# Kernel tuning notes

Hardware: AMD Instinct MI355X
Metric: run time of the kernel (lower is better)

## Reference

```python
import jax, jax.numpy as jnp
import numpy as np


def position_encoding(feature_size, d_model):
    pos = jnp.arange(feature_size, dtype=jnp.float32)[:, None]
    _2i = jnp.arange(0, d_model, 2, dtype=jnp.float32)
    ang = pos / jnp.power(10000.0, _2i / d_model)  # [F, D/2]
    pe = jnp.zeros((feature_size, d_model), dtype=jnp.float32)
    pe = pe.at[:, 0::2].set(jnp.sin(ang))
    pe = pe.at[:, 1::2].set(jnp.cos(ang))
    return pe


def setup_inputs() -> dict:
    key = jax.random.key(0)
    ks = jax.random.split(key, 11)
    B, F, D, T, V = 32, 512, 256, 32, 128
    sc = 0.02
    return {
        "f": jax.random.normal(ks[0], (B, F, D), dtype=jnp.float32),
        "decoder_input_ids": jax.random.randint(ks[1], (B, T), 0, V),
        "emb": sc * jax.random.normal(ks[2], (V, D), dtype=jnp.float32),
        "w_e": sc * jax.random.normal(ks[3], (D, D), dtype=jnp.float32),
        "w_h": sc * jax.random.normal(ks[4], (D, D), dtype=jnp.float32),
        "w_f": sc * jax.random.normal(ks[5], (D, D), dtype=jnp.float32),
        "w_q": sc * jax.random.normal(ks[6], (D, D), dtype=jnp.float32),
        "w_s": sc * jax.random.normal(ks[7], (D, D), dtype=jnp.float32),
        "w_g": sc * jax.random.normal(ks[8], (D, 2 * D), dtype=jnp.float32),
        "w_ih": sc * jax.random.normal(ks[9], (4 * D, 2 * D), dtype=jnp.float32),
        "w_hh": sc * jax.random.normal(ks[10], (4 * D, D), dtype=jnp.float32),
    }


def reference(f, decoder_input_ids, emb, w_e, w_h, w_f, w_q, w_s, w_g, w_ih, w_hh):
    B, F, D = f.shape
    q = position_encoding(F, D)                      # [F, D]
    dec = emb[decoder_input_ids]                     # [B, T, D]
    # loop-invariant attention terms, hoisted: w_f(f) + w_q(q)
    base = jnp.einsum('bfd,od->bfo', f, w_f) + (q @ w_q.T)[None]  # [B, F, D]
    fq = f + q[None]                                 # [B, F, D]

    def step(carry, x_t):
        h, cell, s, cp = carry
        # LSTMCell (bias=False), torch gate order i, f, g, o
        xin = jnp.concatenate([x_t, cp], axis=-1)    # [B, 2D]
        gates = xin @ w_ih.T + h @ w_hh.T            # [B, 4D]
        gi, gf, gg, go = jnp.split(gates, 4, axis=-1)
        cell = jax.nn.sigmoid(gf) * cell + jax.nn.sigmoid(gi) * jnp.tanh(gg)
        h = jax.nn.sigmoid(go) * jnp.tanh(cell)
        # Bahdanau-style energy; softmax over feature (last) dim per source
        t_in = jnp.tanh((h @ w_h.T)[:, None] + base + jnp.einsum('bfd,od->bfo', s, w_s))
        e = jnp.einsum('bfd,od->bfo', t_in, w_e)     # [B, F, D]
        alpha = jax.nn.softmax(e, axis=-1)
        s = s + alpha
        c = (alpha * f).sum(1)                       # [B, D]
        cp = (alpha * fq).sum(1)                     # [B, D]
        pred = jnp.concatenate([c, h], axis=-1) @ w_g.T  # [B, D]
        return (h, cell, s, cp), pred

    z = jnp.zeros((B, D), dtype=f.dtype)
    carry0 = (z, z, jnp.zeros_like(f), z)
    _, preds = jax.lax.scan(step, carry0, jnp.swapaxes(dec, 0, 1))  # [T, B, D]
    return jnp.swapaxes(preds, 0, 1)                 # [B, T, D]
```

## Files before the change

### kernel.cpp

```cpp
#include <hip/hip_runtime.h>
#include <math.h>

#define NB 32
#define NF 512
#define ND 256
#define NT 32
#define RPB 32
#define NTILE (NF / RPB)

typedef __attribute__((ext_vector_type(8))) short bf16x8;
typedef __attribute__((ext_vector_type(4))) float f32x4;

__device__ __forceinline__ float sigmoidf_(float x) { return 1.0f / (1.0f + __expf(-x)); }

__device__ __forceinline__ short f2bf(float x) {
    union { float f; unsigned u; } v; v.f = x;
    unsigned r = (v.u + 0x7FFF + ((v.u >> 16) & 1)) >> 16;
    return (short)r;
}

__global__ void pe_kernel(float* __restrict__ q) {
    int p = blockIdx.x;
    int d = threadIdx.x;
    float i2 = (float)((d >> 1) << 1);
    float rate = expf(-9.210340371976184f * (i2 / (float)ND));
    float ang = (float)p * rate;
    q[p * ND + d] = (d & 1) ? cosf(ang) : sinf(ang);
}

__global__ void gather_kernel(const int* __restrict__ ids, const float* __restrict__ emb,
                              float* __restrict__ dec) {
    int bt = blockIdx.x;
    int d = threadIdx.x;
    dec[(size_t)bt * ND + d] = emb[(size_t)ids[bt] * ND + d];
}

__global__ void wcvt_kernel(const float* __restrict__ w, short* __restrict__ wb, int n) {
    int i = blockIdx.x * 256 + threadIdx.x;
    if (i < n) wb[i] = f2bf(w[i]);
}

__global__ void qwq_kernel(const float* __restrict__ q, const float* __restrict__ w_q,
                           float* __restrict__ qwq) {
    int p = blockIdx.x;
    int o = threadIdx.x;
    __shared__ float qs[ND];
    qs[o] = q[(size_t)p * ND + o];
    __syncthreads();
    const float4* wr = (const float4*)(w_q + (size_t)o * ND);
    float acc = 0.f;
    for (int k4 = 0; k4 < ND / 4; ++k4) {
        float4 w = wr[k4];
        int k = 4 * k4;
        acc += qs[k] * w.x + qs[k + 1] * w.y + qs[k + 2] * w.z + qs[k + 3] * w.w;
    }
    qwq[(size_t)p * ND + o] = acc;
}

__global__ void base_kernel(const float* __restrict__ fin, const float* __restrict__ w_f,
                            const float* __restrict__ qwq, float* __restrict__ bsum) {
    int b = blockIdx.x / NTILE;
    int f0 = (blockIdx.x % NTILE) * RPB;
    int o = threadIdx.x;
    __shared__ float fs[RPB][ND];
    #pragma unroll
    for (int r = 0; r < RPB; ++r)
        fs[r][o] = fin[((size_t)(b * NF + f0 + r)) * ND + o];
    __syncthreads();
    float acc[RPB];
    #pragma unroll
    for (int r = 0; r < RPB; ++r) acc[r] = 0.f;
    const float4* wr = (const float4*)(w_f + (size_t)o * ND);
    for (int k4 = 0; k4 < ND / 4; ++k4) {
        float4 w = wr[k4];
        int k = 4 * k4;
        #pragma unroll
        for (int r = 0; r < RPB; ++r)
            acc[r] += fs[r][k] * w.x + fs[r][k + 1] * w.y + fs[r][k + 2] * w.z + fs[r][k + 3] * w.w;
    }
    #pragma unroll
    for (int r = 0; r < RPB; ++r)
        bsum[((size_t)(b * NF + f0 + r)) * ND + o] = acc[r] + qwq[(size_t)(f0 + r) * ND + o];
}

#define ZSTRIDE 769
#define ZPSTRIDE 513
__global__ void gates_kernel(int t, int mode,
                             const float* __restrict__ dec,
                             const float* __restrict__ cpart, const float* __restrict__ cppart,
                             const float* __restrict__ h,
                             const float* __restrict__ w_ih, const float* __restrict__ w_hh,
                             const float* __restrict__ w_g,
                             float* __restrict__ gatesT, float* __restrict__ out) {
    extern __shared__ float lds[];
    int bid = blockIdx.x;
    int tid = threadIdx.x;

    if (bid < 128) {
        if (!(mode & 1)) return;
        int j0 = bid * 8;
        float* wl = lds;
        float* zl = lds + 8 * 768;
        float4* wl4 = (float4*)wl;
        for (int cc = 0; cc < 6; ++cc) {
            int idx4 = tid + cc * 256;
            int flat = idx4 * 4;
            int r = flat / 768;
            int col = flat - r * 768;
            float4 v;
            if (col < 512) v = *(const float4*)(w_ih + (size_t)(j0 + r) * 512 + col);
            else           v = *(const float4*)(w_hh + (size_t)(j0 + r) * 256 + (col - 512));
            wl4[idx4] = v;
        }
        for (int b = 0; b < NB; ++b) {
            int d = tid;
            float xv = (t < NT) ? dec[((size_t)b * NT + t) * ND + d] : 0.f;
            float cpsum = 0.f;
            if (t > 0) {
                #pragma unroll
                for (int tl = 0; tl < NTILE; ++tl)
                    cpsum += cppart[((size_t)tl * NB + b) * ND + d];
            }
            float hv = h[(size_t)b * ND + d];
            zl[b * ZSTRIDE + d]       = xv;
            zl[b * ZSTRIDE + 256 + d] = cpsum;
            zl[b * ZSTRIDE + 512 + d] = hv;
        }
        __syncthreads();
        int r = tid >> 5;
        int b = tid & 31;
        const float4* wr4 = (const float4*)(wl + r * 768);
        const float* zb = zl + b * ZSTRIDE;
        float acc = 0.f;
        #pragma unroll 8
        for (int k4 = 0; k4 < 192; ++k4) {
            float4 w = wr4[k4];
            int k = 4 * k4;
            acc += w.x * zb[k] + w.y * zb[k + 1] + w.z * zb[k + 2] + w.w * zb[k + 3];
        }
        gatesT[(size_t)b * 1024 + (j0 + r)] = acc;
    } else {
        if (!(mode & 2)) return;
        int p0 = (bid - 128) * 8;
        float* wl = lds;
        float* zl = lds + 8 * 512;
        float4* wl4 = (float4*)wl;
        for (int cc = 0; cc < 4; ++cc) {
            int idx4 = tid + cc * 256;
            int flat = idx4 * 4;
            int r = flat >> 9;
            int col = flat & 511;
            wl4[idx4] = *(const float4*)(w_g + (size_t)(p0 + r) * 512 + col);
        }
        for (int b = 0; b < NB; ++b) {
            float csum = 0.f;
            #pragma unroll
            for (int tl = 0; tl < NTILE; ++tl)
                csum += cpart[((size_t)tl * NB + b) * ND + tid];
            zl[b * ZPSTRIDE + tid]       = csum;
            zl[b * ZPSTRIDE + 256 + tid] = h[(size_t)b * ND + tid];
        }
        __syncthreads();
        int r = tid >> 5;
        int b = tid & 31;
        const float4* wr4 = (const float4*)(wl + r * 512);
        const float* zb = zl + b * ZPSTRIDE;
        float acc = 0.f;
        #pragma unroll 8
        for (int k4 = 0; k4 < 128; ++k4) {
            float4 w = wr4[k4];
            int k = 4 * k4;
            acc += w.x * zb[k] + w.y * zb[k + 1] + w.z * zb[k + 2] + w.w * zb[k + 3];
        }
        out[((size_t)b * NT + (t - 1)) * ND + p0 + r] = acc;
    }
}

__global__ void __launch_bounds__(256) attn_step_kernel(
        float* __restrict__ bsum,
        const float* __restrict__ fin, const float* __restrict__ q,
        const float* __restrict__ gatesT,
        const float* __restrict__ cell_prev, float* __restrict__ cell_next,
        float* __restrict__ h_next,
        const float* __restrict__ w_h,
        const short* __restrict__ w_e_bf, const short* __restrict__ w_s_bf,
        float* __restrict__ cpart, float* __restrict__ cppart) {
    int b = blockIdx.x / NTILE;
    int tile = blockIdx.x % NTILE;
    int f0 = tile * RPB;
    int tid = threadIdx.x;
    int l = tid & 63;
    int wv = tid >> 6;

    __shared__ __align__(16) short tin_bf[RPB * ND];
    __shared__ float xfer[RPB * 257];
    __shared__ float hn[ND];
    __shared__ float sred[RPB][5];

    int o0 = wv * 64;
    int c15 = l & 15;
    int g = l >> 4;
    char* tb = (char*)tin_bf;

    {
        float gi = gatesT[(size_t)b * 1024 + tid];
        float gf = gatesT[(size_t)b * 1024 + 256 + tid];
        float gg = gatesT[(size_t)b * 1024 + 512 + tid];
        float go = gatesT[(size_t)b * 1024 + 768 + tid];
        float cold = cell_prev[(size_t)b * ND + tid];
        float cnew = sigmoidf_(gf) * cold + sigmoidf_(gi) * tanhf(gg);
        float hval = sigmoidf_(go) * tanhf(cnew);
        if (tile == 0) {
            cell_next[(size_t)b * ND + tid] = cnew;
            h_next[(size_t)b * ND + tid] = hval;
        }
        hn[tid] = hval;
    }
    __syncthreads();
    float hwh_reg = 0.f;
    {
        const float4* whr = (const float4*)(w_h + (size_t)tid * ND);
        #pragma unroll 8
        for (int k4 = 0; k4 < ND / 4; ++k4) {
            float4 w = whr[k4]; int k = 4 * k4;
            hwh_reg += hn[k] * w.x + hn[k + 1] * w.y + hn[k + 2] * w.z + hn[k + 3] * w.w;
        }
    }

    float bsv[RPB];
    #pragma unroll
    for (int r = 0; r < RPB; ++r) {
        float bs = bsum[((size_t)(b * NF + f0 + r)) * ND + tid];
        bsv[r] = bs;
        int byte = (r * 512 + tid * 2) ^ ((r & 7) << 4);
        *(short*)(tb + byte) = f2bf(tanhf(hwh_reg + bs));
    }
    __syncthreads();

    f32x4 acc[2][4];
    #pragma unroll
    for (int mt = 0; mt < 2; ++mt)
        #pragma unroll
        for (int nt = 0; nt < 4; ++nt)
            acc[mt][nt] = (f32x4)0.f;
    #pragma unroll
    for (int ks = 0; ks < 8; ++ks) {
        int kb = ks * 32 + g * 8;
        bf16x8 afr[2];
        #pragma unroll
        for (int mt = 0; mt < 2; ++mt) {
            int row = mt * 16 + c15;
            int byte = (row * 512 + kb * 2) ^ ((row & 7) << 4);
            afr[mt] = *(const bf16x8*)(tb + byte);
        }
        #pragma unroll
        for (int nt = 0; nt < 4; ++nt) {
            int o = o0 + nt * 16 + c15;
            bf16x8 bfr = *(const bf16x8*)(w_e_bf + (size_t)o * ND + kb);
            #pragma unroll
            for (int mt = 0; mt < 2; ++mt)
                acc[mt][nt] = __builtin_amdgcn_mfma_f32_16x16x32_bf16(afr[mt], bfr, acc[mt][nt], 0, 0, 0);
        }
    }

    {
        float ps[2][4];
        #pragma unroll
        for (int mt = 0; mt < 2; ++mt)
            #pragma unroll
            for (int reg = 0; reg < 4; ++reg) ps[mt][reg] = 0.f;
        #pragma unroll
        for (int mt = 0; mt < 2; ++mt)
            #pragma unroll
            for (int nt = 0; nt < 4; ++nt)
                #pragma unroll
                for (int reg = 0; reg < 4; ++reg) {
                    float a = __expf(acc[mt][nt][reg]);
                    acc[mt][nt][reg] = a;
                    ps[mt][reg] += a;
                }
        #pragma unroll
        for (int off = 1; off <= 8; off <<= 1)
            #pragma unroll
            for (int mt = 0; mt < 2; ++mt)
                #pragma unroll
                for (int reg = 0; reg < 4; ++reg)
                    ps[mt][reg] += __shfl_xor(ps[mt][reg], off);
        if (c15 == 0) {
            #pragma unroll
            for (int mt = 0; mt < 2; ++mt)
                #pragma unroll
                for (int reg = 0; reg < 4; ++reg)
                    sred[mt * 16 + g * 4 + reg][wv] = ps[mt][reg];
        }
        __syncthreads();
        #pragma unroll
        for (int mt = 0; mt < 2; ++mt)
            #pragma unroll
            for (int reg = 0; reg < 4; ++reg) {
                int r = mt * 16 + g * 4 + reg;
                float inv = 1.0f / (sred[r][0] + sred[r][1] + sred[r][2] + sred[r][3]);
                #pragma unroll
                for (int nt = 0; nt < 4; ++nt)
                    acc[mt][nt][reg] *= inv;
            }
    }

    #pragma unroll
    for (int mt = 0; mt < 2; ++mt)
        #pragma unroll
        for (int reg = 0; reg < 4; ++reg) {
            int r = mt * 16 + g * 4 + reg;
            #pragma unroll
            for (int nt = 0; nt < 4; ++nt)
                xfer[r * 257 + o0 + nt * 16 + c15] = acc[mt][nt][reg];
        }
    __syncthreads();

    {
        float pc = 0.f, pcp = 0.f;
        #pragma unroll
        for (int r = 0; r < RPB; ++r) {
            float a = xfer[r * 257 + tid];
            float fv = fin[((size_t)(b * NF + f0 + r)) * ND + tid];
            float qv = q[(size_t)(f0 + r) * ND + tid];
            pc += a * fv;
            pcp += a * (fv + qv);
            int byte = (r * 512 + tid * 2) ^ ((r & 7) << 4);
            *(short*)(tb + byte) = f2bf(a);
        }
        cpart [((size_t)tile * NB + b) * ND + tid] = pc;
        cppart[((size_t)tile * NB + b) * ND + tid] = pcp;
    }
    __syncthreads();

    {
        f32x4 acc2[2][4];
        #pragma unroll
        for (int mt = 0; mt < 2; ++mt)
            #pragma unroll
            for (int nt = 0; nt < 4; ++nt)
                acc2[mt][nt] = (f32x4)0.f;
        #pragma unroll
        for (int ks = 0; ks < 8; ++ks) {
            int kb = ks * 32 + g * 8;
            bf16x8 afr[2];
            #pragma unroll
            for (int mt = 0; mt < 2; ++mt) {
                int row = mt * 16 + c15;
                int byte = (row * 512 + kb * 2) ^ ((row & 7) << 4);
                afr[mt] = *(const bf16x8*)(tb + byte);
            }
            #pragma unroll
            for (int nt = 0; nt < 4; ++nt) {
                int o = o0 + nt * 16 + c15;
                bf16x8 bfr = *(const bf16x8*)(w_s_bf + (size_t)o * ND + kb);
                #pragma unroll
                for (int mt = 0; mt < 2; ++mt)
                    acc2[mt][nt] = __builtin_amdgcn_mfma_f32_16x16x32_bf16(afr[mt], bfr, acc2[mt][nt], 0, 0, 0);
            }
        }
        #pragma unroll
        for (int mt = 0; mt < 2; ++mt)
            #pragma unroll
            for (int reg = 0; reg < 4; ++reg) {
                int r = mt * 16 + g * 4 + reg;
                #pragma unroll
                for (int nt = 0; nt < 4; ++nt)
                    xfer[r * 257 + o0 + nt * 16 + c15] = acc2[mt][nt][reg];
            }
    }
    __syncthreads();

    #pragma unroll
    for (int r = 0; r < RPB; ++r)
        bsum[((size_t)(b * NF + f0 + r)) * ND + tid] = bsv[r] + xfer[r * 257 + tid];
}

extern "C" void kernel_launch(void* const* d_in, const int* in_sizes, int n_in,
                              void* d_out, int out_size, void* d_ws, size_t ws_size,
                              hipStream_t stream) {
    const float* fin  = (const float*)d_in[0];
    const int*   ids  = (const int*)  d_in[1];
    const float* emb  = (const float*)d_in[2];
    const float* w_e  = (const float*)d_in[3];
    const float* w_h  = (const float*)d_in[4];
    const float* w_f  = (const float*)d_in[5];
    const float* w_q  = (const float*)d_in[6];
    const float* w_s  = (const float*)d_in[7];
    const float* w_g  = (const float*)d_in[8];
    const float* w_ih = (const float*)d_in[9];
    const float* w_hh = (const float*)d_in[10];
    float* out = (float*)d_out;
    float* ws  = (float*)d_ws;

    size_t off = 0;
    float* q      = ws + off; off += (size_t)NF * ND;
    float* scratch= ws + off; off += (size_t)NF * ND;
    float* dec    = ws + off; off += (size_t)NB * NT * ND;
    float* bsum   = ws + off; off += (size_t)NB * NF * ND;
    float* h0     = ws + off; off += (size_t)NB * ND;
    float* h1     = ws + off; off += (size_t)NB * ND;
    float* cell0  = ws + off; off += (size_t)NB * ND;
    float* cell1  = ws + off; off += (size_t)NB * ND;
    float* cpart  = ws + off; off += (size_t)NTILE * NB * ND;
    float* cppart = ws + off; off += (size_t)NTILE * NB * ND;
    short* w_e_bf = (short*)(ws + off); off += (size_t)ND * ND / 2;
    short* w_s_bf = (short*)(ws + off); off += (size_t)ND * ND / 2;

    float* qwq    = scratch;
    float* gatesT = scratch;

    float* hbuf[2]    = { h0, h1 };
    float* cellbuf[2] = { cell0, cell1 };

    hipMemsetAsync(h0, 0, sizeof(float) * NB * ND, stream);
    hipMemsetAsync(cell0, 0, sizeof(float) * NB * ND, stream);

    pe_kernel<<<NF, ND, 0, stream>>>(q);
    gather_kernel<<<NB * NT, ND, 0, stream>>>(ids, emb, dec);
    wcvt_kernel<<<ND * ND / 256, 256, 0, stream>>>(w_e, w_e_bf, ND * ND);
    wcvt_kernel<<<ND * ND / 256, 256, 0, stream>>>(w_s, w_s_bf, ND * ND);
    qwq_kernel<<<NF, ND, 0, stream>>>(q, w_q, qwq);
    base_kernel<<<NB * NTILE, ND, 0, stream>>>(fin, w_f, qwq, bsum);

    const size_t gates_lds = (size_t)(8 * 768 + NB * ZSTRIDE) * sizeof(float);

    for (int t = 0; t < NT; ++t) {
        int mode = (t > 0) ? 3 : 1;
        int p = t & 1;
        gates_kernel<<<160, ND, gates_lds, stream>>>(t, mode, dec, cpart, cppart, hbuf[p],
                                                     w_ih, w_hh, w_g, gatesT, out);
        attn_step_kernel<<<NB * NTILE, ND, 0, stream>>>(bsum, fin, q, gatesT,
                                                        cellbuf[p], cellbuf[p ^ 1], hbuf[p ^ 1],
                                                        w_h, w_e_bf, w_s_bf, cpart, cppart);
    }
    gates_kernel<<<160, ND, gates_lds, stream>>>(NT, 2, dec, cpart, cppart, hbuf[0],
                                                 w_ih, w_hh, w_g, gatesT, out);
}
```

Measured before the change: 2.676 ms.

## Vectorize attention step epilogues, transpose w_h/w_g, restructure output projection and gather

Many changes at once. The embedding gather kernel is removed and the gates kernel reads emb by id directly. w_h and w_g are pre-transposed so h@w_h and the output projection read coalesced columns, and the output-projection blocks now cover one batch row each instead of 8 output rows. The attention step kernel gets float4 loads and stores for bsum, f and q, a 4-wave LDS reduction for the context sums, a padded xfer stride, launch bounds allowing 2 blocks per SM, and a separate gatesT buffer instead of aliasing the qwq scratch. The aim is fewer uncoalesced scalar accesses and higher occupancy, at the cost of more LDS and a few extra syncs.

After: 2.680 ms. No clear change (+0.2%).

```diff
diff --git a/kernel.cpp b/kernel.cpp
--- a/kernel.cpp
+++ b/kernel.cpp
@@ -7,8 +7,10 @@
 #define NT 32
 #define RPB 32
 #define NTILE (NF / RPB)
+#define XS 260
 
 typedef __attribute__((ext_vector_type(8))) short bf16x8;
+typedef __attribute__((ext_vector_type(4))) short bf16x4;
 typedef __attribute__((ext_vector_type(4))) float f32x4;
 
 __device__ __forceinline__ float sigmoidf_(float x) { return 1.0f / (1.0f + __expf(-x)); }
@@ -28,16 +30,17 @@
     q[p * ND + d] = (d & 1) ? cosf(ang) : sinf(ang);
 }
 
-__global__ void gather_kernel(const int* __restrict__ ids, const float* __restrict__ emb,
-                              float* __restrict__ dec) {
-    int bt = blockIdx.x;
-    int d = threadIdx.x;
-    dec[(size_t)bt * ND + d] = emb[(size_t)ids[bt] * ND + d];
-}
-
 __global__ void wcvt_kernel(const float* __restrict__ w, short* __restrict__ wb, int n) {
     int i = blockIdx.x * 256 + threadIdx.x;
     if (i < n) wb[i] = f2bf(w[i]);
+}
+
+__global__ void wprep_kernel(const float* __restrict__ w_h, const float* __restrict__ w_g,
+                             float* __restrict__ w_hT, float* __restrict__ w_gT) {
+    int k = blockIdx.x;
+    int o = threadIdx.x;
+    if (k < ND) w_hT[(size_t)k * ND + o] = w_h[(size_t)o * ND + k];
+    w_gT[(size_t)k * ND + o] = w_g[(size_t)o * 512 + k];
 }
 
 __global__ void qwq_kernel(const float* __restrict__ q, const float* __restrict__ w_q,
@@ -84,13 +87,12 @@
 }
 
 #define ZSTRIDE 769
-#define ZPSTRIDE 513
 __global__ void gates_kernel(int t, int mode,
-                             const float* __restrict__ dec,
+                             const int* __restrict__ ids, const float* __restrict__ emb,
                              const float* __restrict__ cpart, const float* __restrict__ cppart,
                              const float* __restrict__ h,
                              const float* __restrict__ w_ih, const float* __restrict__ w_hh,
-                             const float* __restrict__ w_g,
+                             const float* __restrict__ w_gT,
                              float* __restrict__ gatesT, float* __restrict__ out) {
     extern __shared__ float lds[];
     int bid = blockIdx.x;
@@ -114,7 +116,7 @@
         }
         for (int b = 0; b < NB; ++b) {
             int d = tid;
-            float xv = (t < NT) ? dec[((size_t)b * NT + t) * ND + d] : 0.f;
+            float xv = (t < NT) ? emb[(size_t)ids[b * NT + t] * ND + d] : 0.f;
             float cpsum = 0.f;
             if (t > 0) {
                 #pragma unroll
@@ -141,48 +143,30 @@
         gatesT[(size_t)b * 1024 + (j0 + r)] = acc;
     } else {
         if (!(mode & 2)) return;
-        int p0 = (bid - 128) * 8;
-        float* wl = lds;
-        float* zl = lds + 8 * 512;
-        float4* wl4 = (float4*)wl;
-        for (int cc = 0; cc < 4; ++cc) {
-            int idx4 = tid + cc * 256;
-            int flat = idx4 * 4;
-            int r = flat >> 9;
-            int col = flat & 511;
-            wl4[idx4] = *(const float4*)(w_g + (size_t)(p0 + r) * 512 + col);
-        }
-        for (int b = 0; b < NB; ++b) {
-            float csum = 0.f;
-            #pragma unroll
-            for (int tl = 0; tl < NTILE; ++tl)
-                csum += cpart[((size_t)tl * NB + b) * ND + tid];
-            zl[b * ZPSTRIDE + tid]       = csum;
-            zl[b * ZPSTRIDE + 256 + tid] = h[(size_t)b * ND + tid];
-        }
+        int b = bid - 128;
+        float* zp = lds;
+        float csum = 0.f;
+        #pragma unroll
+        for (int tl = 0; tl < NTILE; ++tl)
+            csum += cpart[((size_t)tl * NB + b) * ND + tid];
+        zp[tid] = csum;
+        zp[256 + tid] = h[(size_t)b * ND + tid];
         __syncthreads();
-        int r = tid >> 5;
-        int b = tid & 31;
-        const float4* wr4 = (const float4*)(wl + r * 512);
-        const float* zb = zl + b * ZPSTRIDE;
-        float acc = 0.f;
+        float p = 0.f;
         #pragma unroll 8
-        for (int k4 = 0; k4 < 128; ++k4) {
-            float4 w = wr4[k4];
-            int k = 4 * k4;
-            acc += w.x * zb[k] + w.y * zb[k + 1] + w.z * zb[k + 2] + w.w * zb[k + 3];
-        }
-        out[((size_t)b * NT + (t - 1)) * ND + p0 + r] = acc;
-    }
-}
-
-__global__ void __launch_bounds__(256) attn_step_kernel(
+        for (int k = 0; k < 512; ++k)
+            p += zp[k] * w_gT[(size_t)k * ND + tid];
+        out[((size_t)b * NT + (t - 1)) * ND + tid] = p;
+    }
+}
+
+__global__ void __launch_bounds__(256, 2) attn_step_kernel(
         float* __restrict__ bsum,
-        const float* __restrict__ fin, const float* __restrict__ q,
+        const float* __restrict__ fin, const float* __restrict__ qpe,
         const float* __restrict__ gatesT,
         const float* __restrict__ cell_prev, float* __restrict__ cell_next,
         float* __restrict__ h_next,
-        const float* __restrict__ w_h,
+        const float* __restrict__ w_hT,
         const short* __restrict__ w_e_bf, const short* __restrict__ w_s_bf,
         float* __restrict__ cpart, float* __restrict__ cppart) {
     int b = blockIdx.x / NTILE;
@@ -191,16 +175,18 @@
     int tid = threadIdx.x;
     int l = tid & 63;
     int wv = tid >> 6;
-
-    __shared__ __align__(16) short tin_bf[RPB * ND];
-    __shared__ float xfer[RPB * 257];
-    __shared__ float hn[ND];
-    __shared__ float sred[RPB][5];
-
-    int o0 = wv * 64;
     int c15 = l & 15;
     int g = l >> 4;
+    int c = l;
+    int o0 = wv * 64;
+
+    __shared__ __align__(16) short tin_bf[RPB * ND];
+    __shared__ float xfer[RPB * XS];
+    __shared__ float cred[2][1024];
+    __shared__ float sred[RPB][5];
     char* tb = (char*)tin_bf;
+    float* hn = xfer;
+    float* hwhl = xfer + 256;
 
     {
         float gi = gatesT[(size_t)b * 1024 + tid];
@@ -217,23 +203,29 @@
         hn[tid] = hval;
     }
     __syncthreads();
-    float hwh_reg = 0.f;
-    {
-        const float4* whr = (const float4*)(w_h + (size_t)tid * ND);
+    {
+        float a = 0.f;
         #pragma unroll 8
-        for (int k4 = 0; k4 < ND / 4; ++k4) {
-            float4 w = whr[k4]; int k = 4 * k4;
-            hwh_reg += hn[k] * w.x + hn[k + 1] * w.y + hn[k + 2] * w.z + hn[k + 3] * w.w;
-        }
-    }
-
-    float bsv[RPB];
-    #pragma unroll
-    for (int r = 0; r < RPB; ++r) {
-        float bs = bsum[((size_t)(b * NF + f0 + r)) * ND + tid];
-        bsv[r] = bs;
-        int byte = (r * 512 + tid * 2) ^ ((r & 7) << 4);
-        *(short*)(tb + byte) = f2bf(tanhf(hwh_reg + bs));
+        for (int k = 0; k < ND; ++k)
+            a += hn[k] * w_hT[(size_t)k * ND + tid];
+        hwhl[tid] = a;
+    }
+    __syncthreads();
+
+    float4 bsv4[8];
+    {
+        float4 hwh4 = *(const float4*)&hwhl[4 * c];
+        #pragma unroll
+        for (int i = 0; i < 8; ++i) {
+            int r = wv + 4 * i;
+            bsv4[i] = *(const float4*)(bsum + ((size_t)(b * NF + f0 + r)) * ND + 4 * c);
+            bf16x4 tv;
+            tv.x = f2bf(tanhf(hwh4.x + bsv4[i].x));
+            tv.y = f2bf(tanhf(hwh4.y + bsv4[i].y));
+            tv.z = f2bf(tanhf(hwh4.z + bsv4[i].z));
+            tv.w = f2bf(tanhf(hwh4.w + bsv4[i].w));
+            *(bf16x4*)(tb + ((r * 512 + 8 * c) ^ ((r & 7) << 4))) = tv;
+        }
     }
     __syncthreads();
 
@@ -250,8 +242,7 @@
         #pragma unroll
         for (int mt = 0; mt < 2; ++mt) {
             int row = mt * 16 + c15;
-            int byte = (row * 512 + kb * 2) ^ ((row & 7) << 4);
-            afr[mt] = *(const bf16x8*)(tb + byte);
+            afr[mt] = *(const bf16x8*)(tb + ((row * 512 + kb * 2) ^ ((row & 7) << 4)));
         }
         #pragma unroll
         for (int nt = 0; nt < 4; ++nt) {
@@ -313,26 +304,37 @@
             int r = mt * 16 + g * 4 + reg;
             #pragma unroll
             for (int nt = 0; nt < 4; ++nt)
-                xfer[r * 257 + o0 + nt * 16 + c15] = acc[mt][nt][reg];
-        }
-    __syncthreads();
-
-    {
-        float pc = 0.f, pcp = 0.f;
-        #pragma unroll
-        for (int r = 0; r < RPB; ++r) {
-            float a = xfer[r * 257 + tid];
-            float fv = fin[((size_t)(b * NF + f0 + r)) * ND + tid];
-            float qv = q[(size_t)(f0 + r) * ND + tid];
-            pc += a * fv;
-            pcp += a * (fv + qv);
-            int byte = (r * 512 + tid * 2) ^ ((r & 7) << 4);
-            *(short*)(tb + byte) = f2bf(a);
-        }
+                xfer[r * XS + o0 + nt * 16 + c15] = acc[mt][nt][reg];
+        }
+    __syncthreads();
+
+    {
+        float4 pc4 = {0.f, 0.f, 0.f, 0.f}, pcp4 = {0.f, 0.f, 0.f, 0.f};
+        #pragma unroll
+        for (int i = 0; i < 8; ++i) {
+            int r = wv + 4 * i;
+            float4 a4 = *(const float4*)&xfer[r * XS + 4 * c];
+            float4 f4 = *(const float4*)(fin + ((size_t)(b * NF + f0 + r)) * ND + 4 * c);
+            float4 q4 = *(const float4*)(qpe + ((size_t)(f0 + r)) * ND + 4 * c);
+            pc4.x += a4.x * f4.x;  pcp4.x += a4.x * (f4.x + q4.x);
+            pc4.y += a4.y * f4.y;  pcp4.y += a4.y * (f4.y + q4.y);
+            pc4.z += a4.z * f4.z;  pcp4.z += a4.z * (f4.z + q4.z);
+            pc4.w += a4.w * f4.w;  pcp4.w += a4.w * (f4.w + q4.w);
+            bf16x4 av;
+            av.x = f2bf(a4.x); av.y = f2bf(a4.y); av.z = f2bf(a4.z); av.w = f2bf(a4.w);
+            *(bf16x4*)(tb + ((r * 512 + 8 * c) ^ ((r & 7) << 4))) = av;
+        }
+        *(float4*)&cred[0][wv * 256 + 4 * c] = pc4;
+        *(float4*)&cred[1][wv * 256 + 4 * c] = pcp4;
+    }
+    __syncthreads();
+
+    {
+        float pc  = cred[0][tid] + cred[0][256 + tid] + cred[0][512 + tid] + cred[0][768 + tid];
+        float pcp = cred[1][tid] + cred[1][256 + tid] + cred[1][512 + tid] + cred[1][768 + tid];
         cpart [((size_t)tile * NB + b) * ND + tid] = pc;
         cppart[((size_t)tile * NB + b) * ND + tid] = pcp;
     }
-    __syncthreads();
 
     {
         f32x4 acc2[2][4];
@@ -348,8 +350,7 @@
             #pragma unroll
             for (int mt = 0; mt < 2; ++mt) {
                 int row = mt * 16 + c15;
-                int byte = (row * 512 + kb * 2) ^ ((row & 7) << 4);
-                afr[mt] = *(const bf16x8*)(tb + byte);
+                afr[mt] = *(const bf16x8*)(tb + ((row * 512 + kb * 2) ^ ((row & 7) << 4)));
             }
             #pragma unroll
             for (int nt = 0; nt < 4; ++nt) {
@@ -360,6 +361,7 @@
                     acc2[mt][nt] = __builtin_amdgcn_mfma_f32_16x16x32_bf16(afr[mt], bfr, acc2[mt][nt], 0, 0, 0);
             }
         }
+        __syncthreads();
         #pragma unroll
         for (int mt = 0; mt < 2; ++mt)
             #pragma unroll
@@ -367,14 +369,22 @@
                 int r = mt * 16 + g * 4 + reg;
                 #pragma unroll
                 for (int nt = 0; nt < 4; ++nt)
-                    xfer[r * 257 + o0 + nt * 16 + c15] = acc2[mt][nt][reg];
+                    xfer[r * XS + o0 + nt * 16 + c15] = acc2[mt][nt][reg];
             }
     }
     __syncthreads();
 
     #pragma unroll
-    for (int r = 0; r < RPB; ++r)
-        bsum[((size_t)(b * NF + f0 + r)) * ND + tid] = bsv[r] + xfer[r * 257 + tid];
+    for (int i = 0; i < 8; ++i) {
+        int r = wv + 4 * i;
+        float4 x4 = *(const float4*)&xfer[r * XS + 4 * c];
+        float4 o4;
+        o4.x = bsv4[i].x + x4.x;
+        o4.y = bsv4[i].y + x4.y;
+        o4.z = bsv4[i].z + x4.z;
+        o4.w = bsv4[i].w + x4.w;
+        *(float4*)(bsum + ((size_t)(b * NF + f0 + r)) * ND + 4 * c) = o4;
+    }
 }
 
 extern "C" void kernel_launch(void* const* d_in, const int* in_sizes, int n_in,
@@ -396,21 +406,20 @@
 
     size_t off = 0;
     float* q      = ws + off; off += (size_t)NF * ND;
-    float* scratch= ws + off; off += (size_t)NF * ND;
-    float* dec    = ws + off; off += (size_t)NB * NT * ND;
+    float* qwq    = ws + off; off += (size_t)NF * ND;
     float* bsum   = ws + off; off += (size_t)NB * NF * ND;
     float* h0     = ws + off; off += (size_t)NB * ND;
     float* h1     = ws + off; off += (size_t)NB * ND;
     float* cell0  = ws + off; off += (size_t)NB * ND;
     float* cell1  = ws + off; off += (size_t)NB * ND;
+    float* gatesT = ws + off; off += (size_t)NB * 1024;
     float* cpart  = ws + off; off += (size_t)NTILE * NB * ND;
     float* cppart = ws + off; off += (size_t)NTILE * NB * ND;
+    float* w_hT   = ws + off; off += (size_t)ND * ND;
+    float* w_gT   = ws + off; off += (size_t)512 * ND;
     short* w_e_bf = (short*)(ws + off); off += (size_t)ND * ND / 2;
     short* w_s_bf = (short*)(ws + off); off += (size_t)ND * ND / 2;
 
-    float* qwq    = scratch;
-    float* gatesT = scratch;
-
     float* hbuf[2]    = { h0, h1 };
     float* cellbuf[2] = { cell0, cell1 };
 
@@ -418,9 +427,9 @@
     hipMemsetAsync(cell0, 0, sizeof(float) * NB * ND, stream);
 
     pe_kernel<<<NF, ND, 0, stream>>>(q);
-    gather_kernel<<<NB * NT, ND, 0, stream>>>(ids, emb, dec);
     wcvt_kernel<<<ND * ND / 256, 256, 0, stream>>>(w_e, w_e_bf, ND * ND);
     wcvt_kernel<<<ND * ND / 256, 256, 0, stream>>>(w_s, w_s_bf, ND * ND);
+    wprep_kernel<<<512, ND, 0, stream>>>(w_h, w_g, w_hT, w_gT);
     qwq_kernel<<<NF, ND, 0, stream>>>(q, w_q, qwq);
     base_kernel<<<NB * NTILE, ND, 0, stream>>>(fin, w_f, qwq, bsum);
 
@@ -429,12 +438,12 @@
     for (int t = 0; t < NT; ++t) {
         int mode = (t > 0) ? 3 : 1;
         int p = t & 1;
-        gates_kernel<<<160, ND, gates_lds, stream>>>(t, mode, dec, cpart, cppart, hbuf[p],
-                                                     w_ih, w_hh, w_g, gatesT, out);
+        gates_kernel<<<160, ND, gates_lds, stream>>>(t, mode, ids, emb, cpart, cppart, hbuf[p],
+                                                     w_ih, w_hh, w_gT, gatesT, out);
         attn_step_kernel<<<NB * NTILE, ND, 0, stream>>>(bsum, fin, q, gatesT,
                                                         cellbuf[p], cellbuf[p ^ 1], hbuf[p ^ 1],
-                                                        w_h, w_e_bf, w_s_bf, cpart, cppart);
-    }
-    gates_kernel<<<160, ND, gates_lds, stream>>>(NT, 2, dec, cpart, cppart, hbuf[0],
-                                                 w_ih, w_hh, w_g, gatesT, out);
-}
+                                                        w_hT, w_e_bf, w_s_bf, cpart, cppart);
+    }
+    gates_kernel<<<160, ND, gates_lds, stream>>>(NT, 2, ids, emb, cpart, cppart, hbuf[0],
+                                                 w_ih, w_hh, w_gT, gatesT, out);
+}
```
